# Kernel optimization log

Hardware: AMD Instinct MI355X
Metric: run time of the kernel (lower is better)

Reference implementation:

```python
import jax, jax.numpy as jnp
import numpy as np

D, H, HD, F, L, V, R = 4096, 32, 128, 11008, 2, 32002, 64
ALPHA = 16.0
B, S = 2, 1024
EPS = 1e-5


def setup_inputs() -> dict:
    key = jax.random.key(0)
    ks = jax.random.split(key, 24)
    n = lambda k, shape: (jax.random.normal(k, shape, jnp.float32) * 0.02)
    return {
        "input_ids": jax.random.randint(ks[0], (B, S), 0, V),
        "attention_mask": jnp.ones((B, S), jnp.int32),
        "embed": n(ks[1], (V, D)),
        "Wq": n(ks[2], (L, D, D)), "Wk": n(ks[3], (L, D, D)),
        "Wv": n(ks[4], (L, D, D)), "Wo": n(ks[5], (L, D, D)),
        "Aq": n(ks[6], (L, R, D)), "Bq": jnp.zeros((L, D, R), jnp.float32),
        "Ak": n(ks[7], (L, R, D)), "Bk": n(ks[8], (L, D, R)),
        "Av": n(ks[9], (L, R, D)), "Bv": n(ks[10], (L, D, R)),
        "Ao": n(ks[11], (L, R, D)), "Bo": n(ks[12], (L, D, R)),
        "Wgate": n(ks[13], (L, F, D)), "Wup": n(ks[14], (L, F, D)),
        "Wdown": n(ks[15], (L, D, F)),
        "attn_norm_w": jnp.ones((L, D), jnp.float32),
        "mlp_norm_w": jnp.ones((L, D), jnp.float32),
        "final_norm_w": jnp.ones((D,), jnp.float32),
        "cls_W": n(ks[16], (3, D)), "cls_b": jnp.zeros((3,), jnp.float32),
    }


def _rmsnorm(x, w):
    var = jnp.mean(jnp.square(x), axis=-1, keepdims=True)
    return (x * jax.lax.rsqrt(var + EPS)) * w


def _rope(seq_len):
    inv = 1.0 / (10000.0 ** (jnp.arange(0, HD, 2, dtype=jnp.float32) / HD))
    freqs = jnp.outer(jnp.arange(seq_len, dtype=jnp.float32), inv)  # [S, HD/2]
    emb = jnp.concatenate([freqs, freqs], -1)  # [S, HD]
    return jnp.cos(emb), jnp.sin(emb)


def _rot_half(x):
    h = x.shape[-1] // 2
    return jnp.concatenate([-x[..., h:], x[..., :h]], -1)


def _lora(h, W, A, Bm):
    # h @ W.T + (alpha/r) * (h @ A.T) @ B.T   (dropout inactive in eval)
    return h @ W.T + (h @ A.T) @ Bm.T * (ALPHA / R)


def reference(input_ids, attention_mask, embed, Wq, Wk, Wv, Wo,
              Aq, Bq, Ak, Bk, Av, Bv, Ao, Bo,
              Wgate, Wup, Wdown, attn_norm_w, mlp_norm_w, final_norm_w,
              cls_W, cls_b):
    b, s = input_ids.shape
    x = embed[input_ids]  # [B,S,D]
    cos, sin = _rope(s)  # [S,HD]
    causal = jnp.tril(jnp.ones((s, s), bool))
    mask = causal[None, None] & (attention_mask[:, None, None, :] > 0)
    bias = jnp.where(mask, 0.0, -1e9).astype(jnp.float32)  # [B,1,S,S]

    def heads(t):  # [B,S,D] -> [B,H,S,HD]
        return t.reshape(b, s, H, HD).transpose(0, 2, 1, 3)

    for l in range(L):
        h = _rmsnorm(x, attn_norm_w[l])
        q = heads(_lora(h, Wq[l], Aq[l], Bq[l]))
        k = heads(_lora(h, Wk[l], Ak[l], Bk[l]))
        v = heads(_lora(h, Wv[l], Av[l], Bv[l]))
        q = q * cos + _rot_half(q) * sin
        k = k * cos + _rot_half(k) * sin
        scores = jnp.einsum('bhqd,bhkd->bhqk', q, k) / np.sqrt(HD) + bias
        attn = jax.nn.softmax(scores, axis=-1)
        o = jnp.einsum('bhqk,bhkd->bhqd', attn, v)
        o = o.transpose(0, 2, 1, 3).reshape(b, s, D)
        x = x + _lora(o, Wo[l], Ao[l], Bo[l])
        h = _rmsnorm(x, mlp_norm_w[l])
        x = x + (jax.nn.silu(h @ Wgate[l].T) * (h @ Wup[l].T)) @ Wdown[l].T

    x = _rmsnorm(x, final_norm_w)
    cls = x[:, 0, :]  # [CLS] at position 0 (right padding)
    return cls @ cls_W.T + cls_b
```

## Files before the change

kernel.cpp:

```cpp
#include <hip/hip_runtime.h>
#include <cstdint>
#include <cstddef>

#define D_   4096
#define H_   32
#define HD_  128
#define F_   11008
#define L_   2
#define R_   64
#define BB   2
#define SS   1024
#define TOK  (BB*SS)
#define N3   12288
#define EPS_ 1e-5f

typedef __attribute__((ext_vector_type(8))) short          s16x8;
typedef __attribute__((ext_vector_type(4))) float          fx4;
typedef __attribute__((ext_vector_type(4))) unsigned short u16x4t;
typedef __attribute__((ext_vector_type(8))) unsigned short u16x8t;

__device__ __forceinline__ unsigned short f2bf(float f) {
  union { float f; unsigned u; } x; x.f = f;
  unsigned r = (x.u + 0x7FFFu + ((x.u >> 16) & 1u)) >> 16;
  return (unsigned short)r;
}
__device__ __forceinline__ float b2f(unsigned short h) {
  union { unsigned u; float f; } x; x.u = ((unsigned)h) << 16;
  return x.f;
}

__device__ __forceinline__ void xcd_remap(int nwg, int mt_cnt, int& mt, int& nt) {
  const int orig = blockIdx.x;
  const int q = nwg >> 3, r = nwg & 7;
  const int xcd = orig & 7, i = orig >> 3;
  const int wgid = (xcd < r ? xcd * (q + 1) : r * (q + 1) + (xcd - r) * q) + i;
  mt = wgid % mt_cnt;
  nt = wgid / mt_cnt;
}

__global__ void k_embed(const int* __restrict__ ids, const float* __restrict__ emb,
                        float* __restrict__ x) {
  const int tok = blockIdx.x, tid = threadIdx.x;
  const int id = ids[tok];
  const float* s = emb + (size_t)id * D_;
  float* d = x + (size_t)tok * D_;
#pragma unroll
  for (int i = 0; i < 4; ++i)
    *(fx4*)(d + i * 1024 + tid * 4) = *(const fx4*)(s + i * 1024 + tid * 4);
}

__global__ __launch_bounds__(256) void k_cvt(const float* __restrict__ src,
                                             unsigned short* __restrict__ dst, int n) {
  const int stride = gridDim.x * 256 * 8;
  for (int i = (blockIdx.x * 256 + threadIdx.x) * 8; i < n; i += stride) {
    fx4 a = *(const fx4*)(src + i);
    fx4 b = *(const fx4*)(src + i + 4);
    u16x8t p;
    p[0] = f2bf(a[0]); p[1] = f2bf(a[1]); p[2] = f2bf(a[2]); p[3] = f2bf(a[3]);
    p[4] = f2bf(b[0]); p[5] = f2bf(b[1]); p[6] = f2bf(b[2]); p[7] = f2bf(b[3]);
    *(u16x8t*)(dst + i) = p;
  }
}

__global__ __launch_bounds__(256) void k_rmsnorm(const float* __restrict__ x,
                                                 const float* __restrict__ w,
                                                 unsigned short* __restrict__ out) {
  const int row = blockIdx.x, tid = threadIdx.x;
  const float* xr = x + (size_t)row * D_;
  fx4 v[4];
  float ss = 0.f;
#pragma unroll
  for (int i = 0; i < 4; ++i) {
    v[i] = *(const fx4*)(xr + i * 1024 + tid * 4);
    ss += v[i][0]*v[i][0] + v[i][1]*v[i][1] + v[i][2]*v[i][2] + v[i][3]*v[i][3];
  }
#pragma unroll
  for (int off = 32; off > 0; off >>= 1) ss += __shfl_down(ss, off);
  __shared__ float red[4];
  if ((tid & 63) == 0) red[tid >> 6] = ss;
  __syncthreads();
  const float sc = rsqrtf((red[0] + red[1] + red[2] + red[3]) * (1.f / D_) + EPS_);
  unsigned short* orow = out + (size_t)row * D_;
#pragma unroll
  for (int i = 0; i < 4; ++i) {
    fx4 wv = *(const fx4*)(w + i * 1024 + tid * 4);
    u16x4t pk;
    pk.x = f2bf(v[i][0] * sc * wv[0]);
    pk.y = f2bf(v[i][1] * sc * wv[1]);
    pk.z = f2bf(v[i][2] * sc * wv[2]);
    pk.w = f2bf(v[i][3] * sc * wv[3]);
    *(u16x4t*)(orow + i * 1024 + tid * 4) = pk;
  }
}

template <int NFRAG>
__global__ __launch_bounds__(256, 2) void k_lmid(const unsigned short* __restrict__ Ain,
                                                 const float* __restrict__ P0,
                                                 const float* __restrict__ P1,
                                                 const float* __restrict__ P2,
                                                 float* __restrict__ part) {
  __shared__ unsigned short sA[64 * 64];
  __shared__ unsigned short sW[NFRAG * 16 * 72];
  const int tid = threadIdx.x, wave = tid >> 6, lane = tid & 63;
  const int l15 = lane & 15, l4 = lane >> 4;
  const int m0 = blockIdx.x * 64;
  const int kbase = blockIdx.y * 512;
  const int arow = tid >> 3;
  const int acol = (((tid & 7) ^ (arow & 7)) << 3);
  const int brow = tid >> 4;
  const int bcol = (tid & 15) << 2;
  const float* ptrs[3] = {P0, P1, P2};

  fx4 acc[NFRAG];
#pragma unroll
  for (int j = 0; j < NFRAG; ++j) acc[j] = (fx4){0.f, 0.f, 0.f, 0.f};

  for (int t = 0; t < 8; ++t) {
    const int kb = kbase + t * 64;
#pragma unroll
    for (int i = 0; i < 2; ++i) {
      const unsigned short* gp = Ain + (size_t)(m0 + i * 32 + arow) * 4096 + kb + acol;
      unsigned short* lp = sA + i * 2048 + wave * 512;
      __builtin_amdgcn_global_load_lds(
          (const __attribute__((address_space(1))) unsigned int*)gp,
          (__attribute__((address_space(3))) unsigned int*)lp, 16, 0, 0);
    }
#pragma unroll
    for (int j = 0; j < NFRAG; ++j) {
      const float* wp = ptrs[j >> 2] + (size_t)((j & 3) * 16 + brow) * 4096 + kb + bcol;
      fx4 v = *(const fx4*)wp;
      u16x4t pk;
      pk.x = f2bf(v[0]); pk.y = f2bf(v[1]); pk.z = f2bf(v[2]); pk.w = f2bf(v[3]);
      *(u16x4t*)&sW[(j * 16 + brow) * 72 + bcol] = pk;
    }
    __syncthreads();
#pragma unroll
    for (int ks = 0; ks < 2; ++ks) {
      const int row = wave * 16 + l15;
      const int cid = (((ks * 4) + l4) ^ (row & 7)) << 3;
      s16x8 af = *(const s16x8*)&sA[row * 64 + cid];
#pragma unroll
      for (int j = 0; j < NFRAG; ++j) {
        s16x8 bf = *(const s16x8*)&sW[(j * 16 + l15) * 72 + ks * 32 + (l4 << 3)];
        acc[j] = __builtin_amdgcn_mfma_f32_16x16x32_bf16(af, bf, acc[j], 0, 0, 0);
      }
    }
    __syncthreads();
  }
  const size_t base = (size_t)blockIdx.y * 2048 * (NFRAG * 16);
#pragma unroll
  for (int j = 0; j < NFRAG; ++j)
#pragma unroll
    for (int r = 0; r < 4; ++r)
      part[base + (size_t)(m0 + wave * 16 + l4 * 4 + r) * (NFRAG * 16) + j * 16 + l15] = acc[j][r];
}

__global__ void k_lmred(const float* __restrict__ part, unsigned short* __restrict__ outb, int ld) {
  const int idx = blockIdx.x * 256 + threadIdx.x;
  const int stride = 2048 * ld;
  float s = 0.f;
#pragma unroll
  for (int ks = 0; ks < 8; ++ks) s += part[(size_t)ks * stride + idx];
  outb[idx] = f2bf(0.25f * s);
}

template <int EPI, bool EXT>
__global__ __launch_bounds__(256, 4) void k_gemm(const unsigned short* __restrict__ A,
                                                 const unsigned short* __restrict__ Wb,
                                                 float* __restrict__ outF,
                                                 unsigned short* __restrict__ outB,
                                                 const float* __restrict__ auxF,
                                                 const unsigned short* __restrict__ Aext,
                                                 int ldaE,
                                                 const unsigned short* __restrict__ Wext,
                                                 int M, int N, int K, int nwg) {
  __shared__ unsigned short sA[128 * 64];
  __shared__ unsigned short sB[128 * 64];
  const int tid = threadIdx.x;
  const int wave = tid >> 6, lane = tid & 63;
  int mt, nt;
  xcd_remap(nwg, M >> 7, mt, nt);
  const int m0 = mt * 128, n0 = nt * 128;
  const int wr = wave >> 1, wc = wave & 1;
  const int l15 = lane & 15, l4 = lane >> 4;

  fx4 acc[4][4];
#pragma unroll
  for (int i = 0; i < 4; ++i)
#pragma unroll
    for (int j = 0; j < 4; ++j) acc[i][j] = (fx4){0.f, 0.f, 0.f, 0.f};

  const int nsteps = K >> 6;
  const int arow = tid >> 3;
  const int acol = (((tid & 7) ^ (arow & 7)) << 3);

  for (int t = 0; t < nsteps; ++t) {
    const int kb = t << 6;
#pragma unroll
    for (int i = 0; i < 4; ++i) {
      const unsigned short* gp = A + (size_t)(m0 + i * 32 + arow) * K + kb + acol;
      unsigned short* lp = sA + i * 2048 + wave * 512;
      __builtin_amdgcn_global_load_lds(
          (const __attribute__((address_space(1))) unsigned int*)gp,
          (__attribute__((address_space(3))) unsigned int*)lp, 16, 0, 0);
    }
#pragma unroll
    for (int i = 0; i < 4; ++i) {
      const unsigned short* gp = Wb + (size_t)(n0 + i * 32 + arow) * K + kb + acol;
      unsigned short* lp = sB + i * 2048 + wave * 512;
      __builtin_amdgcn_global_load_lds(
          (const __attribute__((address_space(1))) unsigned int*)gp,
          (__attribute__((address_space(3))) unsigned int*)lp, 16, 0, 0);
    }
    __syncthreads();
#pragma unroll
    for (int ks = 0; ks < 2; ++ks) {
      s16x8 af[4], bfr[4];
#pragma unroll
      for (int i = 0; i < 4; ++i) {
        int row = wr * 64 + i * 16 + l15;
        int cid = (((ks * 4) + l4) ^ (row & 7)) << 3;
        af[i] = *(const s16x8*)&sA[row * 64 + cid];
      }
#pragma unroll
      for (int j = 0; j < 4; ++j) {
        int row = wc * 64 + j * 16 + l15;
        int cid = (((ks * 4) + l4) ^ (row & 7)) << 3;
        bfr[j] = *(const s16x8*)&sB[row * 64 + cid];
      }
#pragma unroll
      for (int i = 0; i < 4; ++i)
#pragma unroll
        for (int j = 0; j < 4; ++j)
          acc[i][j] = __builtin_amdgcn_mfma_f32_16x16x32_bf16(af[i], bfr[j], acc[i][j], 0, 0, 0);
    }
    __syncthreads();
  }

  if constexpr (EXT) {
    const int third = n0 >> 12;
    const unsigned short* Ae = Aext + third * 64;
    const unsigned short* We = Wext + (size_t)n0 * 64;
#pragma unroll
    for (int i = 0; i < 4; ++i) {
      const unsigned short* gp = Ae + (size_t)(m0 + i * 32 + arow) * ldaE + acol;
      unsigned short* lp = sA + i * 2048 + wave * 512;
      __builtin_amdgcn_global_load_lds(
          (const __attribute__((address_space(1))) unsigned int*)gp,
          (__attribute__((address_space(3))) unsigned int*)lp, 16, 0, 0);
    }
#pragma unroll
    for (int i = 0; i < 4; ++i) {
      const unsigned short* gp = We + (size_t)(i * 32 + arow) * 64 + acol;
      unsigned short* lp = sB + i * 2048 + wave * 512;
      __builtin_amdgcn_global_load_lds(
          (const __attribute__((address_space(1))) unsigned int*)gp,
          (__attribute__((address_space(3))) unsigned int*)lp, 16, 0, 0);
    }
    __syncthreads();
#pragma unroll
    for (int ks = 0; ks < 2; ++ks) {
      s16x8 af[4], bfr[4];
#pragma unroll
      for (int i = 0; i < 4; ++i) {
        int row = wr * 64 + i * 16 + l15;
        int cid = (((ks * 4) + l4) ^ (row & 7)) << 3;
        af[i] = *(const s16x8*)&sA[row * 64 + cid];
      }
#pragma unroll
      for (int j = 0; j < 4; ++j) {
        int row = wc * 64 + j * 16 + l15;
        int cid = (((ks * 4) + l4) ^ (row & 7)) << 3;
        bfr[j] = *(const s16x8*)&sB[row * 64 + cid];
      }
#pragma unroll
      for (int i = 0; i < 4; ++i)
#pragma unroll
        for (int j = 0; j < 4; ++j)
          acc[i][j] = __builtin_amdgcn_mfma_f32_16x16x32_bf16(af[i], bfr[j], acc[i][j], 0, 0, 0);
    }
  }

  const int r0 = m0 + wr * 64 + (l4 << 2);
  const int c0 = n0 + wc * 64 + l15;
#pragma unroll
  for (int i = 0; i < 4; ++i)
#pragma unroll
    for (int j = 0; j < 4; ++j)
#pragma unroll
      for (int r = 0; r < 4; ++r) {
        size_t idx = (size_t)(r0 + i * 16 + r) * N + (c0 + j * 16);
        float v = acc[i][j][r];
        if (EPI == 2) outF[idx] = v + auxF[idx];
        else          outB[idx] = f2bf(v);
      }
}

__global__ __launch_bounds__(256, 2) void k_gemm_gu2(const unsigned short* __restrict__ A,
                                                     const unsigned short* __restrict__ Wg,
                                                     const unsigned short* __restrict__ Wu,
                                                     unsigned short* __restrict__ outB,
                                                     int M, int N, int K, int nwg) {
  __shared__ unsigned short sA[128 * 64];
  __shared__ unsigned short sG[128 * 64];
  __shared__ unsigned short sU[128 * 64];
  const int tid = threadIdx.x;
  const int wave = tid >> 6, lane = tid & 63;
  int mt, nt;
  xcd_remap(nwg, M >> 7, mt, nt);
  const int m0 = mt * 128, n0 = nt * 128;
  const int wr = wave >> 1, wc = wave & 1;
  const int l15 = lane & 15, l4 = lane >> 4;

  fx4 accg[4][4], accu[4][4];
#pragma unroll
  for (int i = 0; i < 4; ++i)
#pragma unroll
    for (int j = 0; j < 4; ++j) {
      accg[i][j] = (fx4){0.f, 0.f, 0.f, 0.f};
      accu[i][j] = (fx4){0.f, 0.f, 0.f, 0.f};
    }

  const int nsteps = K >> 6;
  const int arow = tid >> 3;
  const int acol = (((tid & 7) ^ (arow & 7)) << 3);

  for (int t = 0; t < nsteps; ++t) {
    const int kb = t << 6;
#pragma unroll
    for (int i = 0; i < 4; ++i) {
      const unsigned short* gp = A + (size_t)(m0 + i * 32 + arow) * K + kb + acol;
      unsigned short* lp = sA + i * 2048 + wave * 512;
      __builtin_amdgcn_global_load_lds(
          (const __attribute__((address_space(1))) unsigned int*)gp,
          (__attribute__((address_space(3))) unsigned int*)lp, 16, 0, 0);
    }
#pragma unroll
    for (int i = 0; i < 4; ++i) {
      const unsigned short* gp = Wg + (size_t)(n0 + i * 32 + arow) * K + kb + acol;
      unsigned short* lp = sG + i * 2048 + wave * 512;
      __builtin_amdgcn_global_load_lds(
          (const __attribute__((address_space(1))) unsigned int*)gp,
          (__attribute__((address_space(3))) unsigned int*)lp, 16, 0, 0);
    }
#pragma unroll
    for (int i = 0; i < 4; ++i) {
      const unsigned short* gp = Wu + (size_t)(n0 + i * 32 + arow) * K + kb + acol;
      unsigned short* lp = sU + i * 2048 + wave * 512;
      __builtin_amdgcn_global_load_lds(
          (const __attribute__((address_space(1))) unsigned int*)gp,
          (__attribute__((address_space(3))) unsigned int*)lp, 16, 0, 0);
    }
    __syncthreads();
#pragma unroll
    for (int ks = 0; ks < 2; ++ks) {
      s16x8 af[4], bg[4], bu[4];
#pragma unroll
      for (int i = 0; i < 4; ++i) {
        int row = wr * 64 + i * 16 + l15;
        int cid = (((ks * 4) + l4) ^ (row & 7)) << 3;
        af[i] = *(const s16x8*)&sA[row * 64 + cid];
      }
#pragma unroll
      for (int j = 0; j < 4; ++j) {
        int row = wc * 64 + j * 16 + l15;
        int cid = (((ks * 4) + l4) ^ (row & 7)) << 3;
        bg[j] = *(const s16x8*)&sG[row * 64 + cid];
        bu[j] = *(const s16x8*)&sU[row * 64 + cid];
      }
#pragma unroll
      for (int i = 0; i < 4; ++i)
#pragma unroll
        for (int j = 0; j < 4; ++j) {
          accg[i][j] = __builtin_amdgcn_mfma_f32_16x16x32_bf16(af[i], bg[j], accg[i][j], 0, 0, 0);
          accu[i][j] = __builtin_amdgcn_mfma_f32_16x16x32_bf16(af[i], bu[j], accu[i][j], 0, 0, 0);
        }
    }
    __syncthreads();
  }

  const int r0 = m0 + wr * 64 + (l4 << 2);
  const int c0 = n0 + wc * 64 + l15;
#pragma unroll
  for (int i = 0; i < 4; ++i)
#pragma unroll
    for (int j = 0; j < 4; ++j)
#pragma unroll
      for (int r = 0; r < 4; ++r) {
        size_t idx = (size_t)(r0 + i * 16 + r) * N + (c0 + j * 16);
        float g = accg[i][j][r];
        outB[idx] = f2bf(accu[i][j][r] * g / (1.f + __expf(-g)));
      }
}

__global__ void k_ropetab(float* __restrict__ cosT, float* __restrict__ sinT) {
  int idx = blockIdx.x * 256 + threadIdx.x;
  int s = idx >> 6, d = idx & 63;
  float inv = powf(10000.f, -(float)d * (1.f / 64.f));
  float f = (float)s * inv;
  cosT[idx] = cosf(f);
  sinT[idx] = sinf(f);
}

__global__ __launch_bounds__(256, 3) void k_attn(const unsigned short* __restrict__ P3,
                                                 const float* __restrict__ cosT,
                                                 const float* __restrict__ sinT,
                                                 const int* __restrict__ am,
                                                 unsigned short* __restrict__ O) {
  __shared__ unsigned short sK[64 * 136];
  __shared__ unsigned short sV[128 * 72];
  __shared__ unsigned short sP[4 * 16 * 72];
  const int tid = threadIdx.x, wave = tid >> 6, lane = tid & 63;
  const int bh = blockIdx.y, b = bh >> 5, h = bh & 31;
  const int qt = (int)gridDim.x - 1 - blockIdx.x;
  const float scale = 0.08838834764831845f;
  const int l15 = lane & 15, l4 = lane >> 4;

  const int qs = qt * 64 + wave * 16 + l15;
  s16x8 qf[4];
  {
    const unsigned short* qp = P3 + (size_t)(b * SS + qs) * N3 + h * HD_;
    const float* cr = cosT + qs * 64;
    const float* sr = sinT + qs * 64;
#pragma unroll
    for (int ks = 0; ks < 2; ++ks) {
      int dlo = ks * 32 + l4 * 8;
      u16x8t qlo = *(const u16x8t*)(qp + dlo);
      u16x8t qhi = *(const u16x8t*)(qp + dlo + 64);
      u16x8t plo, phi;
#pragma unroll
      for (int j = 0; j < 8; ++j) {
        float lo = b2f(qlo[j]), hi = b2f(qhi[j]);
        float c = cr[dlo + j], s = sr[dlo + j];
        plo[j] = f2bf(lo * c - hi * s);
        phi[j] = f2bf(hi * c + lo * s);
      }
      qf[ks]     = *(s16x8*)&plo;
      qf[ks + 2] = *(s16x8*)&phi;
    }
  }

  fx4 oacc[8];
#pragma unroll
  for (int nf = 0; nf < 8; ++nf) oacc[nf] = (fx4){0.f, 0.f, 0.f, 0.f};
  float mrun[4] = {-1e30f, -1e30f, -1e30f, -1e30f};
  float lrun[4] = {0.f, 0.f, 0.f, 0.f};

  const int ntiles = qt + 1;
  for (int kt = 0; kt < ntiles; ++kt) {
    const int k0 = kt * 64;
    __syncthreads();
    {
      int row = tid >> 2, part = tid & 3;
      int ksr = k0 + row;
      const unsigned short* kp = P3 + (size_t)(b * SS + ksr) * N3 + 4096 + h * HD_;
      const float* cr = cosT + ksr * 64;
      const float* sr = sinT + ksr * 64;
#pragma unroll
      for (int g = 0; g < 2; ++g) {
        int d0 = part * 16 + g * 8;
        u16x8t klo = *(const u16x8t*)(kp + d0);
        u16x8t khi = *(const u16x8t*)(kp + d0 + 64);
        u16x8t wlo, whi;
#pragma unroll
        for (int j = 0; j < 8; ++j) {
          float lo = b2f(klo[j]), hi = b2f(khi[j]);
          float c = cr[d0 + j], s = sr[d0 + j];
          wlo[j] = f2bf(lo * c - hi * s);
          whi[j] = f2bf(hi * c + lo * s);
        }
        *(u16x8t*)&sK[row * 136 + d0]      = wlo;
        *(u16x8t*)&sK[row * 136 + d0 + 64] = whi;
      }
    }
    {
#pragma unroll
      for (int it = 0; it < 8; ++it) {
        int key = it * 8 + (tid >> 5), hd0 = (tid & 31) * 4;
        u16x4t v = *(const u16x4t*)(P3 + (size_t)(b * SS + k0 + key) * N3 + 8192 + h * HD_ + hd0);
        sV[(hd0 + 0) * 72 + key] = v.x;
        sV[(hd0 + 1) * 72 + key] = v.y;
        sV[(hd0 + 2) * 72 + key] = v.z;
        sV[(hd0 + 3) * 72 + key] = v.w;
      }
    }
    __syncthreads();
    if (k0 <= qt * 64 + wave * 16 + 15) {
      fx4 sfr[4];
#pragma unroll
      for (int kf = 0; kf < 4; ++kf) sfr[kf] = (fx4){0.f, 0.f, 0.f, 0.f};
#pragma unroll
      for (int kf = 0; kf < 4; ++kf)
#pragma unroll
        for (int ks = 0; ks < 4; ++ks) {
          s16x8 kfr = *(const s16x8*)&sK[(kf * 16 + l15) * 136 + ks * 32 + l4 * 8];
          sfr[kf] = __builtin_amdgcn_mfma_f32_16x16x32_bf16(qf[ks], kfr, sfr[kf], 0, 0, 0);
        }
      float p[16], corr[4];
#pragma unroll
      for (int r = 0; r < 4; ++r) {
        int qr = qt * 64 + wave * 16 + l4 * 4 + r;
        float mx = -1e30f;
#pragma unroll
        for (int kf = 0; kf < 4; ++kf) {
          int key = k0 + kf * 16 + l15;
          float bb = (key <= qr && am[b * SS + key] != 0) ? 0.f : -1e9f;
          p[kf * 4 + r] = sfr[kf][r] * scale + bb;
          mx = fmaxf(mx, p[kf * 4 + r]);
        }
        mx = fmaxf(mx, __shfl_xor(mx, 1));
        mx = fmaxf(mx, __shfl_xor(mx, 2));
        mx = fmaxf(mx, __shfl_xor(mx, 4));
        mx = fmaxf(mx, __shfl_xor(mx, 8));
        float mn = fmaxf(mrun[r], mx);
        corr[r] = __expf(mrun[r] - mn);
        mrun[r] = mn;
        float rs = 0.f;
#pragma unroll
        for (int kf = 0; kf < 4; ++kf) {
          p[kf * 4 + r] = __expf(p[kf * 4 + r] - mn);
          rs += p[kf * 4 + r];
        }
        rs += __shfl_xor(rs, 1);
        rs += __shfl_xor(rs, 2);
        rs += __shfl_xor(rs, 4);
        rs += __shfl_xor(rs, 8);
        lrun[r] = lrun[r] * corr[r] + rs;
      }
#pragma unroll
      for (int nf = 0; nf < 8; ++nf) {
        oacc[nf][0] *= corr[0];
        oacc[nf][1] *= corr[1];
        oacc[nf][2] *= corr[2];
        oacc[nf][3] *= corr[3];
      }
      unsigned short* pp = sP + wave * (16 * 72);
#pragma unroll
      for (int r = 0; r < 4; ++r) {
        int row = l4 * 4 + r;
#pragma unroll
        for (int kf = 0; kf < 4; ++kf)
          pp[row * 72 + kf * 16 + l15] = f2bf(p[kf * 4 + r]);
      }
      s16x8 pa0 = *(const s16x8*)&pp[l15 * 72 + l4 * 8];
      s16x8 pa1 = *(const s16x8*)&pp[l15 * 72 + 32 + l4 * 8];
#pragma unroll
      for (int nf = 0; nf < 8; ++nf) {
        s16x8 v0 = *(const s16x8*)&sV[(nf * 16 + l15) * 72 + l4 * 8];
        s16x8 v1 = *(const s16x8*)&sV[(nf * 16 + l15) * 72 + 32 + l4 * 8];
        oacc[nf] = __builtin_amdgcn_mfma_f32_16x16x32_bf16(pa0, v0, oacc[nf], 0, 0, 0);
        oacc[nf] = __builtin_amdgcn_mfma_f32_16x16x32_bf16(pa1, v1, oacc[nf], 0, 0, 0);
      }
    }
  }
  const size_t obase = (size_t)b * SS * D_ + h * HD_;
#pragma unroll
  for (int nf = 0; nf < 8; ++nf)
#pragma unroll
    for (int r = 0; r < 4; ++r) {
      int qr = qt * 64 + wave * 16 + l4 * 4 + r;
      O[obase + (size_t)qr * D_ + nf * 16 + l15] = f2bf(oacc[nf][r] / lrun[r]);
    }
}

__global__ __launch_bounds__(256) void k_final(const float* __restrict__ xf,
                                               const float* __restrict__ fw,
                                               const float* __restrict__ cW,
                                               const float* __restrict__ cb,
                                               float* __restrict__ out) {
  const int b = blockIdx.x, tid = threadIdx.x;
  const float* xr = xf + (size_t)b * SS * D_;
  __shared__ float red[4];
  fx4 v[4];
  float ss = 0.f;
#pragma unroll
  for (int i = 0; i < 4; ++i) {
    v[i] = *(const fx4*)(xr + i * 1024 + tid * 4);
    ss += v[i][0]*v[i][0] + v[i][1]*v[i][1] + v[i][2]*v[i][2] + v[i][3]*v[i][3];
  }
#pragma unroll
  for (int off = 32; off > 0; off >>= 1) ss += __shfl_down(ss, off);
  if ((tid & 63) == 0) red[tid >> 6] = ss;
  __syncthreads();
  const float sc = rsqrtf((red[0] + red[1] + red[2] + red[3]) * (1.f / D_) + EPS_);
  for (int c = 0; c < 3; ++c) {
    float d = 0.f;
#pragma unroll
    for (int i = 0; i < 4; ++i) {
      fx4 fv = *(const fx4*)(fw + i * 1024 + tid * 4);
      fx4 cw = *(const fx4*)(cW + (size_t)c * D_ + i * 1024 + tid * 4);
#pragma unroll
      for (int j = 0; j < 4; ++j) d += v[i][j] * sc * fv[j] * cw[j];
    }
#pragma unroll
    for (int off = 32; off > 0; off >>= 1) d += __shfl_down(d, off);
    __syncthreads();
    if ((tid & 63) == 0) red[tid >> 6] = d;
    __syncthreads();
    if (tid == 0) out[b * 3 + c] = red[0] + red[1] + red[2] + red[3] + cb[c];
  }
}

extern "C" void kernel_launch(void* const* d_in, const int* in_sizes, int n_in,
                              void* d_out, int out_size, void* d_ws, size_t ws_size,
                              hipStream_t stream) {
  const int*   ids = (const int*)d_in[0];
  const int*   am  = (const int*)d_in[1];
  const float* emb = (const float*)d_in[2];
  const float* Wq  = (const float*)d_in[3];
  const float* Wk  = (const float*)d_in[4];
  const float* Wv  = (const float*)d_in[5];
  const float* Wo  = (const float*)d_in[6];
  const float* Aq  = (const float*)d_in[7];
  const float* Bq  = (const float*)d_in[8];
  const float* Ak  = (const float*)d_in[9];
  const float* Bk  = (const float*)d_in[10];
  const float* Av  = (const float*)d_in[11];
  const float* Bv  = (const float*)d_in[12];
  const float* Ao  = (const float*)d_in[13];
  const float* Bo  = (const float*)d_in[14];
  const float* Wg  = (const float*)d_in[15];
  const float* Wu  = (const float*)d_in[16];
  const float* Wd  = (const float*)d_in[17];
  const float* anw = (const float*)d_in[18];
  const float* mnw = (const float*)d_in[19];
  const float* fnw = (const float*)d_in[20];
  const float* cW  = (const float*)d_in[21];
  const float* cb  = (const float*)d_in[22];
  float* out = (float*)d_out;

  char* w = (char*)d_ws;
  float* xf = (float*)w;                     w += (size_t)TOK * D_ * 4;
  unsigned short* P3 = (unsigned short*)w;   w += (size_t)TOK * N3 * 2;
  unsigned short* gact = (unsigned short*)w; w += (size_t)TOK * F_ * 2;
  unsigned short* hb = (unsigned short*)w;   w += (size_t)TOK * D_ * 2;
  unsigned short* ob = (unsigned short*)w;   w += (size_t)TOK * D_ * 2;
  unsigned short* Wm3 = (unsigned short*)w;  w += (size_t)3 * D_ * D_ * 2;
  unsigned short* Wgu = (unsigned short*)w;  w += (size_t)2 * F_ * D_ * 2;
  unsigned short* Bx3 = (unsigned short*)w;  w += (size_t)3 * D_ * R_ * 2;
  unsigned short* BxO = (unsigned short*)w;  w += (size_t)D_ * R_ * 2;
  unsigned short* lm3 = (unsigned short*)w;  w += (size_t)TOK * 192 * 2;
  unsigned short* lmo = (unsigned short*)w;  w += (size_t)TOK * 64 * 2;
  float* lm3p = (float*)w;                   w += (size_t)8 * TOK * 192 * 4;
  float* lmop = (float*)w;                   w += (size_t)8 * TOK * 64 * 4;
  float* cosT = (float*)w;                   w += (size_t)SS * 64 * 4;
  float* sinT = (float*)w;                   w += (size_t)SS * 64 * 4;
  if ((size_t)(w - (char*)d_ws) > ws_size) return;

  k_ropetab<<<256, 256, 0, stream>>>(cosT, sinT);
  k_embed<<<TOK, 256, 0, stream>>>(ids, emb, xf);

  const int nwgQKV = (N3 / 128) * (TOK / 128);
  const int nwgProj = (D_ / 128) * (TOK / 128);
  const int nwgMlp = (F_ / 128) * (TOK / 128);
  dim3 gAttn(SS / 64, BB * H_);
  dim3 gLmid(TOK / 64, 8);
  const int CVT_BLK = 2048;

  for (int l = 0; l < L_; ++l) {
    const size_t oDD = (size_t)l * D_ * D_;
    const size_t oRD = (size_t)l * R_ * D_;
    const size_t oDR = (size_t)l * D_ * R_;
    const size_t oFD = (size_t)l * F_ * D_;

    k_rmsnorm<<<TOK, 256, 0, stream>>>(xf, anw + (size_t)l * D_, hb);
    k_cvt<<<CVT_BLK, 256, 0, stream>>>(Wq + oDD, Wm3, D_ * D_);
    k_cvt<<<CVT_BLK, 256, 0, stream>>>(Wk + oDD, Wm3 + (size_t)D_ * D_, D_ * D_);
    k_cvt<<<CVT_BLK, 256, 0, stream>>>(Wv + oDD, Wm3 + (size_t)2 * D_ * D_, D_ * D_);
    k_cvt<<<128, 256, 0, stream>>>(Bq + oDR, Bx3, D_ * R_);
    k_cvt<<<128, 256, 0, stream>>>(Bk + oDR, Bx3 + (size_t)D_ * R_, D_ * R_);
    k_cvt<<<128, 256, 0, stream>>>(Bv + oDR, Bx3 + (size_t)2 * D_ * R_, D_ * R_);
    k_lmid<12><<<gLmid, 256, 0, stream>>>(hb, Aq + oRD, Ak + oRD, Av + oRD, lm3p);
    k_lmred<<<TOK * 192 / 256, 256, 0, stream>>>(lm3p, lm3, 192);
    k_gemm<5, true><<<nwgQKV, 256, 0, stream>>>(hb, Wm3, nullptr, P3, nullptr,
                                                lm3, 192, Bx3, TOK, N3, D_, nwgQKV);
    k_attn<<<gAttn, 256, 0, stream>>>(P3, cosT, sinT, am, ob);
    k_cvt<<<CVT_BLK, 256, 0, stream>>>(Wo + oDD, Wm3, D_ * D_);
    k_cvt<<<128, 256, 0, stream>>>(Bo + oDR, BxO, D_ * R_);
    k_lmid<4><<<gLmid, 256, 0, stream>>>(ob, Ao + oRD, Ao + oRD, Ao + oRD, lmop);
    k_lmred<<<TOK * 64 / 256, 256, 0, stream>>>(lmop, lmo, 64);
    k_gemm<2, true><<<nwgProj, 256, 0, stream>>>(ob, Wm3, xf, nullptr, xf,
                                                 lmo, 64, BxO, TOK, D_, D_, nwgProj);
    k_rmsnorm<<<TOK, 256, 0, stream>>>(xf, mnw + (size_t)l * D_, hb);
    k_cvt<<<CVT_BLK, 256, 0, stream>>>(Wg + oFD, Wgu, F_ * D_);
    k_cvt<<<CVT_BLK, 256, 0, stream>>>(Wu + oFD, Wgu + (size_t)F_ * D_, F_ * D_);
    k_gemm_gu2<<<nwgMlp, 256, 0, stream>>>(hb, Wgu, Wgu + (size_t)F_ * D_, gact, TOK, F_, D_, nwgMlp);
    k_cvt<<<CVT_BLK, 256, 0, stream>>>(Wd + oFD, Wgu, D_ * F_);
    k_gemm<2, false><<<nwgProj, 256, 0, stream>>>(gact, Wgu, xf, nullptr, xf,
                                                  nullptr, 0, nullptr, TOK, D_, F_, nwgProj);
  }

  k_final<<<BB, 256, 0, stream>>>(xf, fnw, cW, cb, out);
  (void)in_sizes; (void)n_in; (void)out_size;
}
```

Measured before the change: 2.875 ms.

## Precompute roped K and transposed V, stream tiles into LDS with swizzle

Adds a prep kernel that applies RoPE to K once and writes V transposed into contiguous per-head buffers. The attention kernel then loads K/V tiles directly into LDS with global_load_lds and an XOR swizzle, replacing the per-tile RoPE recomputation and scalar transposing LDS stores. This removes redundant RoPE work across query tiles (causal reuse) at the cost of an extra kernel launch and extra global traffic to write and reread the K/V buffers.

```diff
diff --git a/kernel.cpp b/kernel.cpp
--- a/kernel.cpp
+++ b/kernel.cpp
@@ -402,13 +402,68 @@
   sinT[idx] = sinf(f);
 }
 
+__global__ __launch_bounds__(256) void k_kvprep(const unsigned short* __restrict__ P3,
+                                                const float* __restrict__ cosT,
+                                                const float* __restrict__ sinT,
+                                                unsigned short* __restrict__ kb,
+                                                unsigned short* __restrict__ vb) {
+  __shared__ unsigned short sT[128 * 72];
+  const int tid = threadIdx.x;
+  const int bh = blockIdx.y, b = bh >> 5, h = bh & 31;
+  const int k0 = blockIdx.x * 64;
+  {
+    int row = tid >> 2, part = tid & 3;
+    int ksr = k0 + row;
+    const unsigned short* kp = P3 + (size_t)(b * SS + ksr) * N3 + 4096 + h * HD_;
+    const float* cr = cosT + ksr * 64;
+    const float* sr = sinT + ksr * 64;
+    unsigned short* kd = kb + ((size_t)bh * SS + ksr) * HD_;
+#pragma unroll
+    for (int g = 0; g < 2; ++g) {
+      int d0 = part * 16 + g * 8;
+      u16x8t klo = *(const u16x8t*)(kp + d0);
+      u16x8t khi = *(const u16x8t*)(kp + d0 + 64);
+      u16x8t wlo, whi;
+#pragma unroll
+      for (int j = 0; j < 8; ++j) {
+        float lo = b2f(klo[j]), hi = b2f(khi[j]);
+        float c = cr[d0 + j], s = sr[d0 + j];
+        wlo[j] = f2bf(lo * c - hi * s);
+        whi[j] = f2bf(hi * c + lo * s);
+      }
+      *(u16x8t*)(kd + d0)      = wlo;
+      *(u16x8t*)(kd + d0 + 64) = whi;
+    }
+  }
+  {
+#pragma unroll
+    for (int it = 0; it < 8; ++it) {
+      int key = it * 8 + (tid >> 5), hd0 = (tid & 31) * 4;
+      u16x4t v = *(const u16x4t*)(P3 + (size_t)(b * SS + k0 + key) * N3 + 8192 + h * HD_ + hd0);
+      sT[(hd0 + 0) * 72 + key] = v.x;
+      sT[(hd0 + 1) * 72 + key] = v.y;
+      sT[(hd0 + 2) * 72 + key] = v.z;
+      sT[(hd0 + 3) * 72 + key] = v.w;
+    }
+    __syncthreads();
+    int hd = tid >> 1, half = tid & 1;
+    unsigned short* vd = vb + ((size_t)bh * HD_ + hd) * SS + k0 + half * 32;
+    const unsigned short* ssrc = sT + hd * 72 + half * 32;
+#pragma unroll
+    for (int j = 0; j < 4; ++j)
+      *(u16x8t*)(vd + j * 8) = *(const u16x8t*)(ssrc + j * 8);
+  }
+}
+
 __global__ __launch_bounds__(256, 3) void k_attn(const unsigned short* __restrict__ P3,
+                                                 const unsigned short* __restrict__ kb,
+                                                 const unsigned short* __restrict__ vb,
                                                  const float* __restrict__ cosT,
                                                  const float* __restrict__ sinT,
                                                  const int* __restrict__ am,
                                                  unsigned short* __restrict__ O) {
-  __shared__ unsigned short sK[64 * 136];
-  __shared__ unsigned short sV[128 * 72];
+  __shared__ unsigned short sK[64 * 128];
+  __shared__ unsigned short sV[128 * 64];
   __shared__ unsigned short sP[4 * 16 * 72];
   const int tid = threadIdx.x, wave = tid >> 6, lane = tid & 63;
   const int bh = blockIdx.y, b = bh >> 5, h = bh & 31;
@@ -440,6 +495,9 @@
     }
   }
 
+  const int krow_l = lane >> 4, kg = lane & 15;
+  const int vrow_l = lane >> 3, vg = lane & 7;
+
   fx4 oacc[8];
 #pragma unroll
   for (int nf = 0; nf < 8; ++nf) oacc[nf] = (fx4){0.f, 0.f, 0.f, 0.f};
@@ -450,39 +508,23 @@
   for (int kt = 0; kt < ntiles; ++kt) {
     const int k0 = kt * 64;
     __syncthreads();
-    {
-      int row = tid >> 2, part = tid & 3;
-      int ksr = k0 + row;
-      const unsigned short* kp = P3 + (size_t)(b * SS + ksr) * N3 + 4096 + h * HD_;
-      const float* cr = cosT + ksr * 64;
-      const float* sr = sinT + ksr * 64;
-#pragma unroll
-      for (int g = 0; g < 2; ++g) {
-        int d0 = part * 16 + g * 8;
-        u16x8t klo = *(const u16x8t*)(kp + d0);
-        u16x8t khi = *(const u16x8t*)(kp + d0 + 64);
-        u16x8t wlo, whi;
-#pragma unroll
-        for (int j = 0; j < 8; ++j) {
-          float lo = b2f(klo[j]), hi = b2f(khi[j]);
-          float c = cr[d0 + j], s = sr[d0 + j];
-          wlo[j] = f2bf(lo * c - hi * s);
-          whi[j] = f2bf(hi * c + lo * s);
-        }
-        *(u16x8t*)&sK[row * 136 + d0]      = wlo;
-        *(u16x8t*)&sK[row * 136 + d0 + 64] = whi;
-      }
-    }
-    {
-#pragma unroll
-      for (int it = 0; it < 8; ++it) {
-        int key = it * 8 + (tid >> 5), hd0 = (tid & 31) * 4;
-        u16x4t v = *(const u16x4t*)(P3 + (size_t)(b * SS + k0 + key) * N3 + 8192 + h * HD_ + hd0);
-        sV[(hd0 + 0) * 72 + key] = v.x;
-        sV[(hd0 + 1) * 72 + key] = v.y;
-        sV[(hd0 + 2) * 72 + key] = v.z;
-        sV[(hd0 + 3) * 72 + key] = v.w;
-      }
+#pragma unroll
+    for (int i = 0; i < 4; ++i) {
+      int row = (i * 4 + wave) * 4 + krow_l;
+      const unsigned short* gp = kb + ((size_t)bh * SS + k0 + row) * HD_ + ((kg ^ (row & 7)) << 3);
+      unsigned short* lp = sK + (i * 4 + wave) * 512;
+      __builtin_amdgcn_global_load_lds(
+          (const __attribute__((address_space(1))) unsigned int*)gp,
+          (__attribute__((address_space(3))) unsigned int*)lp, 16, 0, 0);
+    }
+#pragma unroll
+    for (int i = 0; i < 4; ++i) {
+      int row = (i * 4 + wave) * 8 + vrow_l;
+      const unsigned short* gp = vb + ((size_t)bh * HD_ + row) * SS + k0 + ((vg ^ (row & 7)) << 3);
+      unsigned short* lp = sV + (i * 4 + wave) * 512;
+      __builtin_amdgcn_global_load_lds(
+          (const __attribute__((address_space(1))) unsigned int*)gp,
+          (__attribute__((address_space(3))) unsigned int*)lp, 16, 0, 0);
     }
     __syncthreads();
     if (k0 <= qt * 64 + wave * 16 + 15) {
@@ -490,12 +532,15 @@
 #pragma unroll
       for (int kf = 0; kf < 4; ++kf) sfr[kf] = (fx4){0.f, 0.f, 0.f, 0.f};
 #pragma unroll
-      for (int kf = 0; kf < 4; ++kf)
+      for (int kf = 0; kf < 4; ++kf) {
+        int row = kf * 16 + l15;
 #pragma unroll
         for (int ks = 0; ks < 4; ++ks) {
-          s16x8 kfr = *(const s16x8*)&sK[(kf * 16 + l15) * 136 + ks * 32 + l4 * 8];
+          int cid = ((ks * 4 + l4) ^ (row & 7)) << 3;
+          s16x8 kfr = *(const s16x8*)&sK[row * 128 + cid];
           sfr[kf] = __builtin_amdgcn_mfma_f32_16x16x32_bf16(qf[ks], kfr, sfr[kf], 0, 0, 0);
         }
+      }
       float p[16], corr[4];
 #pragma unroll
       for (int r = 0; r < 4; ++r) {
@@ -546,8 +591,11 @@
       s16x8 pa1 = *(const s16x8*)&pp[l15 * 72 + 32 + l4 * 8];
 #pragma unroll
       for (int nf = 0; nf < 8; ++nf) {
-        s16x8 v0 = *(const s16x8*)&sV[(nf * 16 + l15) * 72 + l4 * 8];
-        s16x8 v1 = *(const s16x8*)&sV[(nf * 16 + l15) * 72 + 32 + l4 * 8];
+        int row = nf * 16 + l15;
+        int c0s = ((0 * 4 + l4) ^ (row & 7)) << 3;
+        int c1s = ((1 * 4 + l4) ^ (row & 7)) << 3;
+        s16x8 v0 = *(const s16x8*)&sV[row * 64 + c0s];
+        s16x8 v1 = *(const s16x8*)&sV[row * 64 + c1s];
         oacc[nf] = __builtin_amdgcn_mfma_f32_16x16x32_bf16(pa0, v0, oacc[nf], 0, 0, 0);
         oacc[nf] = __builtin_amdgcn_mfma_f32_16x16x32_bf16(pa1, v1, oacc[nf], 0, 0, 0);
       }
@@ -635,6 +683,8 @@
   unsigned short* gact = (unsigned short*)w; w += (size_t)TOK * F_ * 2;
   unsigned short* hb = (unsigned short*)w;   w += (size_t)TOK * D_ * 2;
   unsigned short* ob = (unsigned short*)w;   w += (size_t)TOK * D_ * 2;
+  unsigned short* kbuf = (unsigned short*)w; w += (size_t)TOK * D_ * 2;
+  unsigned short* vbuf = (unsigned short*)w; w += (size_t)TOK * D_ * 2;
   unsigned short* Wm3 = (unsigned short*)w;  w += (size_t)3 * D_ * D_ * 2;
   unsigned short* Wgu = (unsigned short*)w;  w += (size_t)2 * F_ * D_ * 2;
   unsigned short* Bx3 = (unsigned short*)w;  w += (size_t)3 * D_ * R_ * 2;
@@ -654,6 +704,7 @@
   const int nwgProj = (D_ / 128) * (TOK / 128);
   const int nwgMlp = (F_ / 128) * (TOK / 128);
   dim3 gAttn(SS / 64, BB * H_);
+  dim3 gPrep(SS / 64, BB * H_);
   dim3 gLmid(TOK / 64, 8);
   const int CVT_BLK = 2048;
 
@@ -674,7 +725,8 @@
     k_lmred<<<TOK * 192 / 256, 256, 0, stream>>>(lm3p, lm3, 192);
     k_gemm<5, true><<<nwgQKV, 256, 0, stream>>>(hb, Wm3, nullptr, P3, nullptr,
                                                 lm3, 192, Bx3, TOK, N3, D_, nwgQKV);
-    k_attn<<<gAttn, 256, 0, stream>>>(P3, cosT, sinT, am, ob);
+    k_kvprep<<<gPrep, 256, 0, stream>>>(P3, cosT, sinT, kbuf, vbuf);
+    k_attn<<<gAttn, 256, 0, stream>>>(P3, kbuf, vbuf, cosT, sinT, am, ob);
     k_cvt<<<CVT_BLK, 256, 0, stream>>>(Wo + oDD, Wm3, D_ * D_);
     k_cvt<<<128, 256, 0, stream>>>(Bo + oDR, BxO, D_ * R_);
     k_lmid<4><<<gLmid, 256, 0, stream>>>(ob, Ao + oRD, Ao + oRD, Ao + oRD, lmop);
```

New measurement: 2.664 ms. 7.3% less time.
